# Kernel optimization log

Hardware: AMD Instinct MI355X
Metric: run time of the kernel (lower is better)

The kernel has to match this reference:

```python
import jax, jax.numpy as jnp
import numpy as np

N = 20000       # nodes
E = 100000      # edges
STEPS = 4
ND = 128        # node feature dim
ED = 128        # edge feature dim
NIN = 128       # node input dim
EIN = 291       # edge input dim (2 + 17*17)
H = 64          # mpn edge-mlp hidden


def _lin(x, w, b):
    return x @ w + b


def setup_inputs():
    key = jax.random.key(0)
    ks = jax.random.split(key, 16)

    def w(k, i, o):
        return (jax.random.normal(k, (i, o), jnp.float32) / np.float32(np.sqrt(i)))

    d = {}
    d["x"] = jax.random.normal(ks[0], (N, NIN), jnp.float32)
    d["edge_attr"] = jax.random.normal(ks[1], (E, EIN), jnp.float32)
    d["edge_index"] = jax.random.randint(ks[2], (2, E), 0, N, jnp.int32)
    # node embedding MLP: NIN -> 128 -> ND (ReLU between, none after last)
    d["new0"] = w(ks[3], NIN, 128); d["neb0"] = jnp.zeros(128, jnp.float32)
    d["new1"] = w(ks[4], 128, ND); d["neb1"] = jnp.zeros(ND, jnp.float32)
    # edge embedding MLP: EIN -> 64 -> ED
    d["eew0"] = w(ks[5], EIN, 64); d["eeb0"] = jnp.zeros(64, jnp.float32)
    d["eew1"] = w(ks[6], 64, ED); d["eeb1"] = jnp.zeros(ED, jnp.float32)
    # MPN edge MLP (skip=True): 2*(2*ND) + 2*ED = 768 -> 64 -> ED, ReLU after each
    d["mew0"] = w(ks[7], 4 * ND + 2 * ED, H); d["meb0"] = jnp.zeros(H, jnp.float32)
    d["mew1"] = w(ks[8], H, ED); d["meb1"] = jnp.zeros(ED, jnp.float32)
    # MPN node MLP: 2*ND + ED = 384 -> ND, ReLU
    d["mnw0"] = w(ks[9], 2 * ND + ED, ND); d["mnb0"] = jnp.zeros(ND, jnp.float32)
    # classification MLP: ED -> 64 -> 32 -> 1
    d["cw0"] = w(ks[10], ED, 64); d["cb0"] = jnp.zeros(64, jnp.float32)
    d["cw1"] = w(ks[11], 64, 32); d["cb1"] = jnp.zeros(32, jnp.float32)
    d["cw2"] = w(ks[12], 32, 1); d["cb2"] = jnp.zeros(1, jnp.float32)
    return d


def reference(x, edge_attr, edge_index,
              new0, neb0, new1, neb1,
              eew0, eeb0, eew1, eeb1,
              mew0, meb0, mew1, meb1,
              mnw0, mnb0,
              cw0, cb0, cw1, cb1, cw2, cb2):
    relu = jax.nn.relu
    j, i = edge_index[0], edge_index[1]  # j: source, i: target

    nf = _lin(relu(_lin(x, new0, neb0)), new1, neb1)          # [N, ND]
    ef = _lin(relu(_lin(edge_attr, eew0, eeb0)), eew1, eeb1)  # [E, ED]
    nf0, ef0 = nf, ef

    for _ in range(STEPS):
        # skip connections: concat initial features
        nfc = jnp.concatenate([nf0, nf], axis=1)  # [N, 2*ND]
        efc = jnp.concatenate([ef0, ef], axis=1)  # [E, 2*ED]
        x_i = nfc[i]  # [E, 2*ND] target
        x_j = nfc[j]  # [E, 2*ND] source
        # edge update MLP (ReLU after both layers)
        h = relu(_lin(jnp.concatenate([x_i, x_j, efc], axis=1), mew0, meb0))
        ef = relu(_lin(h, mew1, meb1))  # [E, ED]
        # message: mlp_node([x_i, edge_attr_new]) aggregated at target i
        msg = relu(_lin(jnp.concatenate([x_i, ef], axis=1), mnw0, mnb0))  # [E, ND]
        nf = jax.ops.segment_sum(msg, i, num_segments=N)  # [N, ND]

    out = relu(_lin(ef, cw0, cb0))
    out = relu(_lin(out, cw1, cb1))
    out = _lin(out, cw2, cb2)  # [E, 1]
    return out
```

## Files before the change

kernel.cpp:

```cpp
#include <hip/hip_runtime.h>
#include <hip/hip_bf16.h>

#define ND 128
#define ED 128
#define NIN 128
#define EIN 291
#define KPAD 320
#define HH 64
#define TM 32
#define TS 64
#define GSE 768
#define MAXGE 3

typedef __attribute__((ext_vector_type(8))) short short8;
typedef __attribute__((ext_vector_type(4))) float float4_;

__device__ __forceinline__ unsigned short f2bf(float f)
{
    union { float f; unsigned u; } v; v.f = f;
    unsigned u = v.u;
    unsigned r = (u + 0x7FFFu + ((u >> 16) & 1u)) >> 16;
    return (unsigned short)r;
}
__device__ __forceinline__ float bf2f(unsigned short s)
{
    union { unsigned u; float f; } v; v.u = ((unsigned)s) << 16;
    return v.f;
}

template<int T, int KC, int K>
__device__ __forceinline__ void stage_frags(const unsigned short* __restrict__ src,
                                            unsigned short* __restrict__ wreg,
                                            int t, int k0)
{
    constexpr int TOT = T * KC * 64;
#pragma unroll
    for (int it = 0; it < TOT / 256; it++) {
        int idx = it * 256 + t;
        int f = idx >> 6, l = idx & 63;
        int col = (f / KC) * 16 + (l & 15);
        int k = (f % KC) * 32 + ((l >> 4) * 8);
        *(short8*)&wreg[idx * 8] = *(const short8*)&src[(size_t)col * K + k0 + k];
    }
}
#define FRAG(wreg, f, lane) (*(const short8*)&(wreg)[(((f) << 6) + (lane)) * 8])

__global__ __launch_bounds__(256) void zero_k(float* __restrict__ p, int n4)
{
    int idx = blockIdx.x * 256 + threadIdx.x;
    if (idx < n4) ((float4*)p)[idx] = make_float4(0.f, 0.f, 0.f, 0.f);
}

__global__ __launch_bounds__(256) void f2bfz_k(float* __restrict__ src,
                                               unsigned short* __restrict__ dst, int n4)
{
    int idx = blockIdx.x * 256 + threadIdx.x;
    if (idx < n4) {
        float4 v = ((const float4*)src)[idx];
        unsigned lo = (unsigned)f2bf(v.x) | ((unsigned)f2bf(v.y) << 16);
        unsigned hi = (unsigned)f2bf(v.z) | ((unsigned)f2bf(v.w) << 16);
        ((uint2*)dst)[idx] = make_uint2(lo, hi);
        ((float4*)src)[idx] = make_float4(0.f, 0.f, 0.f, 0.f);
    }
}

__global__ __launch_bounds__(256) void wprep_k(
    const float* __restrict__ mew0, const float* __restrict__ mew1, const float* __restrict__ mnw0,
    const float* __restrict__ eew0, const float* __restrict__ eew1, const float* __restrict__ cw0,
    const float* __restrict__ new0, const float* __restrict__ new1,
    unsigned short* __restrict__ w0T, unsigned short* __restrict__ w1T,
    unsigned short* __restrict__ wmT, unsigned short* __restrict__ w0eT,
    unsigned short* __restrict__ w1eT, unsigned short* __restrict__ cw0T,
    unsigned short* __restrict__ w0nT, unsigned short* __restrict__ w1nT)
{
    int idx = blockIdx.x * 256 + threadIdx.x;
    if (idx < 49152) {
        int c = idx / 768, k = idx % 768;
        w0T[idx] = f2bf(mew0[k * 64 + c]);
    } else if (idx < 57344) {
        int j = idx - 49152; int c = j / 64, k = j % 64;
        w1T[j] = f2bf(mew1[k * 128 + c]);
    } else if (idx < 106496) {
        int j = idx - 57344; int c = j / 384, k = j % 384;
        wmT[j] = f2bf(mnw0[k * 128 + c]);
    } else if (idx < 126976) {
        int j = idx - 106496; int c = j / KPAD, k = j % KPAD;
        w0eT[j] = (k < EIN) ? f2bf(eew0[k * 64 + c]) : (unsigned short)0;
    } else if (idx < 135168) {
        int j = idx - 126976; int c = j / 64, k = j % 64;
        w1eT[j] = f2bf(eew1[k * 128 + c]);
    } else if (idx < 143360) {
        int j = idx - 135168; int c = j / 128, k = j % 128;
        cw0T[j] = f2bf(cw0[k * 64 + c]);
    } else if (idx < 159744) {
        int j = idx - 143360; int c = j / 128, k = j % 128;
        w0nT[j] = f2bf(new0[k * 128 + c]);
    } else if (idx < 176128) {
        int j = idx - 159744; int c = j / 128, k = j % 128;
        w1nT[j] = f2bf(new1[k * 128 + c]);
    }
}

__global__ __launch_bounds__(256) void node_embed_k(
    const float* __restrict__ x,
    const unsigned short* __restrict__ w0nT, const float* __restrict__ b0,
    const unsigned short* __restrict__ w1nT, const float* __restrict__ b1,
    unsigned short* __restrict__ nf0_bf, unsigned short* __restrict__ nf_bf, int N)
{
    const int t = threadIdx.x;
    const int n0 = blockIdx.x * TM;
    __shared__ unsigned short wreg[8192];
    __shared__ unsigned short xin[TM][130];
    __shared__ unsigned short h_bf[TM][130];

#pragma unroll
    for (int it = 0; it < 4; it++) {
        int idx = it * 256 + t;
        int r = idx >> 5, c4 = idx & 31;
        int node = n0 + r; if (node >= N) node = N - 1;
        float4 v = *(const float4*)(x + (size_t)node * NIN + c4 * 4);
        unsigned lo = (unsigned)f2bf(v.x) | ((unsigned)f2bf(v.y) << 16);
        unsigned hi = (unsigned)f2bf(v.z) | ((unsigned)f2bf(v.w) << 16);
        *(uint2*)&xin[r][c4 * 4] = make_uint2(lo, hi);
    }

    const int w = t >> 6, lane = t & 63, quad = lane >> 4, n16 = lane & 15;
    const int m = w & 1, nh = w >> 1;

    float4_ acc[4];
#pragma unroll
    for (int q = 0; q < 4; q++) acc[q] = (float4_){0.f, 0.f, 0.f, 0.f};
#pragma unroll
    for (int hf = 0; hf < 2; hf++) {
        stage_frags<8, 2, 128>(w0nT, wreg, t, hf * 64);
        __syncthreads();
#pragma unroll
        for (int kc = 0; kc < 2; kc++) {
            short8 a = *(const short8*)&xin[m * 16 + n16][hf * 64 + kc * 32 + quad * 8];
#pragma unroll
            for (int tt = 0; tt < 4; tt++) {
                short8 b = FRAG(wreg, (nh * 4 + tt) * 2 + kc, lane);
                acc[tt] = __builtin_amdgcn_mfma_f32_16x16x32_bf16(a, b, acc[tt], 0, 0, 0);
            }
        }
        __syncthreads();
    }
#pragma unroll
    for (int tt = 0; tt < 4; tt++) {
        int c = nh * 64 + tt * 16 + n16;
        float bias = b0[c];
#pragma unroll
        for (int r4 = 0; r4 < 4; r4++)
            h_bf[m * 16 + quad * 4 + r4][c] = f2bf(fmaxf(acc[tt][r4] + bias, 0.f));
    }
    __syncthreads();

    float4_ acc2[4];
#pragma unroll
    for (int q = 0; q < 4; q++) acc2[q] = (float4_){0.f, 0.f, 0.f, 0.f};
#pragma unroll
    for (int hf = 0; hf < 2; hf++) {
        stage_frags<8, 2, 128>(w1nT, wreg, t, hf * 64);
        __syncthreads();
#pragma unroll
        for (int kc = 0; kc < 2; kc++) {
            short8 a = *(const short8*)&h_bf[m * 16 + n16][hf * 64 + kc * 32 + quad * 8];
#pragma unroll
            for (int tt = 0; tt < 4; tt++) {
                short8 b = FRAG(wreg, (nh * 4 + tt) * 2 + kc, lane);
                acc2[tt] = __builtin_amdgcn_mfma_f32_16x16x32_bf16(a, b, acc2[tt], 0, 0, 0);
            }
        }
        __syncthreads();
    }
#pragma unroll
    for (int tt = 0; tt < 4; tt++) {
        int c = nh * 64 + tt * 16 + n16;
        float bias = b1[c];
#pragma unroll
        for (int r4 = 0; r4 < 4; r4++) {
            int row = m * 16 + quad * 4 + r4;
            int node = n0 + row;
            if (node < N) {
                unsigned short v = f2bf(acc2[tt][r4] + bias);
                nf0_bf[(size_t)node * ND + c] = v;
                nf_bf[(size_t)node * ND + c] = v;
            }
        }
    }
}

__global__ __launch_bounds__(256, 3) void edge_embed_k(
    const float* __restrict__ ea,
    const unsigned short* __restrict__ w0eT, const float* __restrict__ b0,
    const unsigned short* __restrict__ w1eT, const float* __restrict__ b1,
    unsigned short* __restrict__ ef0_bf, unsigned short* __restrict__ ef_bf,
    int E, int ntiles)
{
    const int t = threadIdx.x;
    __shared__ unsigned short w0reg[10240];
    __shared__ unsigned short w1reg[8192];
    __shared__ unsigned short hsl[4][16 * 66];

    const int w = t >> 6, lane = t & 63, quad = lane >> 4, n16 = lane & 15;

    stage_frags<8, 2, 64>(w1eT, w1reg, t, 0);

    int ng = 0;
    int tile[MAXGE];
#pragma unroll
    for (int g = 0; g < MAXGE; g++) {
        int tl = blockIdx.x + g * GSE;
        if (tl < ntiles) { tile[g] = tl; ng = g + 1; }
        else tile[g] = 0;
    }

    float4_ accL[MAXGE][4];
#pragma unroll
    for (int g = 0; g < MAXGE; g++)
#pragma unroll
        for (int q = 0; q < 4; q++) accL[g][q] = (float4_){0.f, 0.f, 0.f, 0.f};

#pragma unroll
    for (int hf = 0; hf < 2; hf++) {
        __syncthreads();
        stage_frags<4, 5, KPAD>(w0eT, w0reg, t, hf * 160);
        __syncthreads();
#pragma unroll
        for (int g = 0; g < MAXGE; g++) {
            if (g < ng) {
                int e = tile[g] * 64 + w * 16 + n16; if (e >= E) e = E - 1;
                const float* src = ea + (size_t)e * EIN;
#pragma unroll
                for (int kc = 0; kc < 5; kc++) {
                    int k = hf * 160 + kc * 32 + quad * 8;
                    union { short8 s; uint4 u; } av;
                    if (k + 8 <= EIN) {
                        float4 v0 = *(const float4*)(src + k);
                        float4 v1 = *(const float4*)(src + k + 4);
                        av.u.x = (unsigned)f2bf(v0.x) | ((unsigned)f2bf(v0.y) << 16);
                        av.u.y = (unsigned)f2bf(v0.z) | ((unsigned)f2bf(v0.w) << 16);
                        av.u.z = (unsigned)f2bf(v1.x) | ((unsigned)f2bf(v1.y) << 16);
                        av.u.w = (unsigned)f2bf(v1.z) | ((unsigned)f2bf(v1.w) << 16);
                    } else {
                        unsigned short vv[8];
#pragma unroll
                        for (int j = 0; j < 8; j++)
                            vv[j] = (k + j < EIN) ? f2bf(src[k + j]) : (unsigned short)0;
                        av.u.x = (unsigned)vv[0] | ((unsigned)vv[1] << 16);
                        av.u.y = (unsigned)vv[2] | ((unsigned)vv[3] << 16);
                        av.u.z = (unsigned)vv[4] | ((unsigned)vv[5] << 16);
                        av.u.w = (unsigned)vv[6] | ((unsigned)vv[7] << 16);
                    }
#pragma unroll
                    for (int tt = 0; tt < 4; tt++) {
                        short8 b = FRAG(w0reg, tt * 5 + kc, lane);
                        accL[g][tt] = __builtin_amdgcn_mfma_f32_16x16x32_bf16(av.s, b, accL[g][tt], 0, 0, 0);
                    }
                }
            }
        }
    }

#pragma unroll
    for (int g = 0; g < MAXGE; g++) {
        if (g < ng) {
#pragma unroll
            for (int tt = 0; tt < 4; tt++) {
                int c = tt * 16 + n16;
                float bias = b0[c];
#pragma unroll
                for (int r4 = 0; r4 < 4; r4++)
                    hsl[w][(quad * 4 + r4) * 66 + c] = f2bf(fmaxf(accL[g][tt][r4] + bias, 0.f));
            }
            float4_ acc2[8];
#pragma unroll
            for (int q = 0; q < 8; q++) acc2[q] = (float4_){0.f, 0.f, 0.f, 0.f};
#pragma unroll
            for (int kc = 0; kc < 2; kc++) {
                short8 a2 = *(const short8*)&hsl[w][n16 * 66 + kc * 32 + quad * 8];
#pragma unroll
                for (int tt = 0; tt < 8; tt++)
                    acc2[tt] = __builtin_amdgcn_mfma_f32_16x16x32_bf16(
                        a2, FRAG(w1reg, tt * 2 + kc, lane), acc2[tt], 0, 0, 0);
            }
#pragma unroll
            for (int tt = 0; tt < 8; tt++) {
                int c = tt * 16 + n16;
                float bias = b1[c];
#pragma unroll
                for (int r4 = 0; r4 < 4; r4++) {
                    int e = tile[g] * 64 + w * 16 + quad * 4 + r4;
                    if (e < E) {
                        unsigned short v = f2bf(acc2[tt][r4] + bias);
                        ef0_bf[(size_t)e * ED + c] = v;
                        ef_bf[(size_t)e * ED + c] = v;
                    }
                }
            }
        }
    }
}

__global__ __launch_bounds__(256, 3) void edge_step_k(
    const int* __restrict__ srcj, const int* __restrict__ tgti,
    const unsigned short* __restrict__ nf0_bf, const unsigned short* __restrict__ nf_bf,
    const unsigned short* __restrict__ ef0_bf, unsigned short* __restrict__ ef_bf,
    float* __restrict__ nfn,
    const unsigned short* __restrict__ w0T, const float* __restrict__ meb0,
    const unsigned short* __restrict__ w1T, const float* __restrict__ meb1,
    const unsigned short* __restrict__ wmT, const float* __restrict__ mnb0, int E)
{
    const int t = threadIdx.x;
    const int e0 = blockIdx.x * TS;
    __shared__ unsigned short wreg[8192];
    __shared__ unsigned short h_bf[TS][66];
    __shared__ unsigned short efn_bf[TS][130];
    __shared__ int sidx[TS];

    if (t < TS) { int e = e0 + t; if (e >= E) e = E - 1; sidx[t] = tgti[e]; }

    const int w = t >> 6, lane = t & 63, quad = lane >> 4, n16 = lane & 15;
    const int erow = w * 16 + n16;
    int ec = e0 + erow; if (ec >= E) ec = E - 1;
    const int ti = tgti[ec], sj = srcj[ec];

    short8 areg[24];
    {
        const unsigned short* pAs[6] = {
            nf0_bf + (size_t)ti * ND + quad * 8,
            nf_bf  + (size_t)ti * ND + quad * 8,
            nf0_bf + (size_t)sj * ND + quad * 8,
            nf_bf  + (size_t)sj * ND + quad * 8,
            ef0_bf + (size_t)ec * ED + quad * 8,
            ef_bf  + (size_t)ec * ED + quad * 8 };
#pragma unroll
        for (int f = 0; f < 24; f++)
            areg[f] = *(const short8*)(pAs[f >> 2] + (f & 3) * 32);
    }

    float4_ accL[4];
#pragma unroll
    for (int q = 0; q < 4; q++) accL[q] = (float4_){0.f, 0.f, 0.f, 0.f};
#pragma unroll
    for (int hf = 0; hf < 6; hf++) {
        stage_frags<4, 4, 768>(w0T, wreg, t, hf * 128);
        __syncthreads();
#pragma unroll
        for (int kc = 0; kc < 4; kc++) {
#pragma unroll
            for (int tt = 0; tt < 4; tt++) {
                short8 b = FRAG(wreg, tt * 4 + kc, lane);
                accL[tt] = __builtin_amdgcn_mfma_f32_16x16x32_bf16(areg[hf * 4 + kc], b, accL[tt], 0, 0, 0);
            }
        }
        __syncthreads();
    }
#pragma unroll
    for (int tt = 0; tt < 4; tt++) {
        int c = tt * 16 + n16;
        float bias = meb0[c];
#pragma unroll
        for (int r4 = 0; r4 < 4; r4++)
            h_bf[w * 16 + quad * 4 + r4][c] = f2bf(fmaxf(accL[tt][r4] + bias, 0.f));
    }
    __syncthreads();

    stage_frags<8, 2, 64>(w1T, wreg, t, 0);
    __syncthreads();
    {
        float4_ acc[8];
#pragma unroll
        for (int q = 0; q < 8; q++) acc[q] = (float4_){0.f, 0.f, 0.f, 0.f};
#pragma unroll
        for (int kc = 0; kc < 2; kc++) {
            short8 a = *(const short8*)&h_bf[w * 16 + n16][kc * 32 + quad * 8];
#pragma unroll
            for (int tt = 0; tt < 8; tt++) {
                short8 b = FRAG(wreg, tt * 2 + kc, lane);
                acc[tt] = __builtin_amdgcn_mfma_f32_16x16x32_bf16(a, b, acc[tt], 0, 0, 0);
            }
        }
#pragma unroll
        for (int tt = 0; tt < 8; tt++) {
            int c = tt * 16 + n16;
            float bias = meb1[c];
#pragma unroll
            for (int r4 = 0; r4 < 4; r4++) {
                int row = w * 16 + quad * 4 + r4;
                unsigned short v = f2bf(fmaxf(acc[tt][r4] + bias, 0.f));
                efn_bf[row][c] = v;
                int e = e0 + row;
                if (e < E) ef_bf[(size_t)e * ED + c] = v;
            }
        }
    }
    __syncthreads();

    float4_ accM[8];
#pragma unroll
    for (int q = 0; q < 8; q++) accM[q] = (float4_){0.f, 0.f, 0.f, 0.f};
#pragma unroll
    for (int hf = 0; hf < 6; hf++) {
        stage_frags<8, 2, 384>(wmT, wreg, t, hf * 64);
        __syncthreads();
#pragma unroll
        for (int kc = 0; kc < 2; kc++) {
            int kk = hf * 2 + kc;
            short8 a;
            if (kk < 8) a = areg[kk];
            else        a = *(const short8*)&efn_bf[erow][(kk - 8) * 32 + quad * 8];
#pragma unroll
            for (int tt = 0; tt < 8; tt++) {
                short8 b = FRAG(wreg, tt * 2 + kc, lane);
                accM[tt] = __builtin_amdgcn_mfma_f32_16x16x32_bf16(a, b, accM[tt], 0, 0, 0);
            }
        }
        __syncthreads();
    }
#pragma unroll
    for (int tt = 0; tt < 8; tt++) {
        int c = tt * 16 + n16;
        float bias = mnb0[c];
#pragma unroll
        for (int r4 = 0; r4 < 4; r4++) {
            int row = w * 16 + quad * 4 + r4;
            int e = e0 + row;
            if (e < E)
                atomicAdd(&nfn[(size_t)sidx[row] * ND + c],
                          fmaxf(accM[tt][r4] + bias, 0.f));
        }
    }
}

__global__ __launch_bounds__(256) void classify_k(
    const unsigned short* __restrict__ ef_bf,
    const unsigned short* __restrict__ cw0T, const float* __restrict__ cb0,
    const float* __restrict__ cw1, const float* __restrict__ cb1,
    const float* __restrict__ cw2, const float* __restrict__ cb2,
    float* __restrict__ out, int E)
{
    const int t = threadIdx.x;
    const int e0 = blockIdx.x * TM;
    __shared__ unsigned short h0_bf[TM][66];
    __shared__ float h1[TM][33];

    const int w = t >> 6, lane = t & 63, quad = lane >> 4, n16 = lane & 15;
    const int m = w & 1;
    const int erow = m * 16 + n16;
    int ec = e0 + erow; if (ec >= E) ec = E - 1;
    const unsigned short* pa = ef_bf + (size_t)ec * ED + quad * 8;

    {
        const int cb = (w >> 1) * 32;
        float4_ acc0 = {0.f, 0.f, 0.f, 0.f}, acc1 = acc0;
        const unsigned short* b0p = cw0T + (size_t)(cb + n16) * 128 + quad * 8;
        const unsigned short* b1p = b0p + (size_t)16 * 128;
#pragma unroll
        for (int kc = 0; kc < 4; kc++) {
            short8 a  = *(const short8*)(pa + kc * 32);
            short8 bb0 = *(const short8*)(b0p + kc * 32);
            short8 bb1 = *(const short8*)(b1p + kc * 32);
            acc0 = __builtin_amdgcn_mfma_f32_16x16x32_bf16(a, bb0, acc0, 0, 0, 0);
            acc1 = __builtin_amdgcn_mfma_f32_16x16x32_bf16(a, bb1, acc1, 0, 0, 0);
        }
#pragma unroll
        for (int t2 = 0; t2 < 2; t2++) {
            int c = cb + t2 * 16 + n16;
            float bias = cb0[c];
            float4_ ac = t2 ? acc1 : acc0;
#pragma unroll
            for (int r4 = 0; r4 < 4; r4++)
                h0_bf[m * 16 + quad * 4 + r4][c] = f2bf(fmaxf(ac[r4] + bias, 0.f));
        }
    }
    __syncthreads();

    {
        int c = t & 31;
        int rbase = (t >> 5) * 4;
#pragma unroll
        for (int q = 0; q < 4; q++) {
            int r = rbase + q;
            float acc = cb1[c];
#pragma unroll 8
            for (int k = 0; k < 64; k++) acc += bf2f(h0_bf[r][k]) * cw1[k * 32 + c];
            h1[r][c] = fmaxf(acc, 0.f);
        }
    }
    __syncthreads();

    if (t < TM) {
        int e = e0 + t;
        if (e < E) {
            float a = cb2[0];
#pragma unroll
            for (int k = 0; k < 32; k++) a += h1[t][k] * cw2[k];
            out[e] = a;
        }
    }
}

extern "C" void kernel_launch(void* const* d_in, const int* in_sizes, int n_in,
                              void* d_out, int out_size, void* d_ws, size_t ws_size,
                              hipStream_t stream)
{
    const float* x    = (const float*)d_in[0];
    const float* ea   = (const float*)d_in[1];
    const int*   eidx = (const int*)d_in[2];
    const float* new0 = (const float*)d_in[3];  const float* neb0 = (const float*)d_in[4];
    const float* new1 = (const float*)d_in[5];  const float* neb1 = (const float*)d_in[6];
    const float* eew0 = (const float*)d_in[7];  const float* eeb0 = (const float*)d_in[8];
    const float* eew1 = (const float*)d_in[9];  const float* eeb1 = (const float*)d_in[10];
    const float* mew0 = (const float*)d_in[11]; const float* meb0 = (const float*)d_in[12];
    const float* mew1 = (const float*)d_in[13]; const float* meb1 = (const float*)d_in[14];
    const float* mnw0 = (const float*)d_in[15]; const float* mnb0 = (const float*)d_in[16];
    const float* cw0  = (const float*)d_in[17]; const float* cb0  = (const float*)d_in[18];
    const float* cw1  = (const float*)d_in[19]; const float* cb1  = (const float*)d_in[20];
    const float* cw2  = (const float*)d_in[21]; const float* cb2  = (const float*)d_in[22];

    const int N = in_sizes[0] / NIN;
    const int E = in_sizes[2] / 2;
    const int* srcj = eidx;
    const int* tgti = eidx + E;

    char* wsb = (char*)d_ws;
    float* nfn = (float*)wsb;
    unsigned short* nf0_bf = (unsigned short*)(nfn + (size_t)N * ND);
    unsigned short* nf_bf  = nf0_bf + (size_t)N * ND;
    unsigned short* ef0_bf = nf_bf + (size_t)N * ND;
    unsigned short* ef_bf  = ef0_bf + (size_t)E * ED;
    unsigned short* w0T  = ef_bf + (size_t)E * ED;
    unsigned short* w1T  = w0T + 49152;
    unsigned short* wmT  = w1T + 8192;
    unsigned short* w0eT = wmT + 49152;
    unsigned short* w1eT = w0eT + 64 * KPAD;
    unsigned short* cw0T = w1eT + 8192;
    unsigned short* w0nT = cw0T + 8192;
    unsigned short* w1nT = w0nT + 16384;

    const int eblocks32 = (E + TM - 1) / TM;
    const int nblocks32 = (N + TM - 1) / TM;
    const int ntiles64 = (E + 63) / 64;

    wprep_k<<<(176128 + 255) / 256, 256, 0, stream>>>(mew0, mew1, mnw0, eew0, eew1, cw0,
                                                      new0, new1,
                                                      w0T, w1T, wmT, w0eT, w1eT, cw0T,
                                                      w0nT, w1nT);
    node_embed_k<<<nblocks32, 256, 0, stream>>>(x, w0nT, neb0, w1nT, neb1,
                                                nf0_bf, nf_bf, N);
    edge_embed_k<<<GSE, 256, 0, stream>>>(ea, w0eT, eeb0, w1eT, eeb1,
                                          ef0_bf, ef_bf, E, ntiles64);

    const int n4 = (N * ND) / 4;
    const int zgrid = (n4 + 255) / 256;
    zero_k<<<zgrid, 256, 0, stream>>>(nfn, n4);

    for (int s = 0; s < 4; s++) {
        edge_step_k<<<ntiles64, 256, 0, stream>>>(srcj, tgti, nf0_bf, nf_bf,
                                                  ef0_bf, ef_bf, nfn,
                                                  w0T, meb0, w1T, meb1, wmT, mnb0, E);
        f2bfz_k<<<zgrid, 256, 0, stream>>>(nfn, nf_bf, n4);
    }

    classify_k<<<eblocks32, 256, 0, stream>>>(ef_bf, cw0T, cb0, cw1, cb1, cw2, cb2,
                                              (float*)d_out, E);
}
```

Measured before the change: 786.1 us.

## Replace atomic scatter-add with CSR gather aggregation and skip unused final message

Builds a CSR index of edges grouped by target node (histogram, single-block scan, scatter) once per call. The edge step now writes bf16 messages to a buffer, and a separate gather kernel sums each node's incoming messages, replacing fp32 atomicAdd into a node buffer and the convert-and-zero pass. The last step skips the node-message MLP entirely, since its aggregate is never used by the classifier. The cost is an extra message round-trip through memory, a serial single-block scan, and bf16 rounding of messages before summation.

```diff
diff --git a/kernel.cpp b/kernel.cpp
--- a/kernel.cpp
+++ b/kernel.cpp
@@ -51,17 +51,65 @@
     if (idx < n4) ((float4*)p)[idx] = make_float4(0.f, 0.f, 0.f, 0.f);
 }
 
-__global__ __launch_bounds__(256) void f2bfz_k(float* __restrict__ src,
-                                               unsigned short* __restrict__ dst, int n4)
-{
-    int idx = blockIdx.x * 256 + threadIdx.x;
-    if (idx < n4) {
-        float4 v = ((const float4*)src)[idx];
-        unsigned lo = (unsigned)f2bf(v.x) | ((unsigned)f2bf(v.y) << 16);
-        unsigned hi = (unsigned)f2bf(v.z) | ((unsigned)f2bf(v.w) << 16);
-        ((uint2*)dst)[idx] = make_uint2(lo, hi);
-        ((float4*)src)[idx] = make_float4(0.f, 0.f, 0.f, 0.f);
-    }
+__global__ __launch_bounds__(256) void hist_k(const int* __restrict__ tgti,
+                                              int* __restrict__ deg, int E)
+{
+    int e = blockIdx.x * 256 + threadIdx.x;
+    if (e < E) atomicAdd(&deg[tgti[e]], 1);
+}
+
+__global__ __launch_bounds__(256) void scan_k(const int* __restrict__ deg,
+                                              int* __restrict__ row_ptr,
+                                              int* __restrict__ cursor, int N, int E)
+{
+    __shared__ int part[256];
+    const int t = threadIdx.x;
+    const int chunk = (N + 255) / 256;
+    const int base = t * chunk;
+    int s = 0;
+    for (int k = 0; k < chunk; k++) { int idx = base + k; if (idx < N) s += deg[idx]; }
+    part[t] = s;
+    __syncthreads();
+    for (int off = 1; off < 256; off <<= 1) {
+        int v = (t >= off) ? part[t - off] : 0;
+        __syncthreads();
+        part[t] += v;
+        __syncthreads();
+    }
+    int run = (t == 0) ? 0 : part[t - 1];
+    for (int k = 0; k < chunk; k++) {
+        int idx = base + k;
+        if (idx < N) { row_ptr[idx] = run; cursor[idx] = run; run += deg[idx]; }
+    }
+    if (t == 255) row_ptr[N] = E;
+}
+
+__global__ __launch_bounds__(256) void scatter_k(const int* __restrict__ tgti,
+                                                 int* __restrict__ cursor,
+                                                 int* __restrict__ csr_eid, int E)
+{
+    int e = blockIdx.x * 256 + threadIdx.x;
+    if (e < E) {
+        int p = atomicAdd(&cursor[tgti[e]], 1);
+        csr_eid[p] = e;
+    }
+}
+
+__global__ __launch_bounds__(256) void agg_k(const int* __restrict__ row_ptr,
+                                             const int* __restrict__ csr_eid,
+                                             const unsigned short* __restrict__ msg,
+                                             unsigned short* __restrict__ nf_bf, int N)
+{
+    int n = blockIdx.x * 2 + (threadIdx.x >> 7);
+    int c = threadIdx.x & 127;
+    if (n >= N) return;
+    int beg = row_ptr[n], end = row_ptr[n + 1];
+    float acc = 0.f;
+    for (int k = beg; k < end; k++) {
+        int e = csr_eid[k];
+        acc += bf2f(msg[(size_t)e * ND + c]);
+    }
+    nf_bf[(size_t)n * ND + c] = f2bf(acc);
 }
 
 __global__ __launch_bounds__(256) void wprep_k(
@@ -306,19 +354,17 @@
     const int* __restrict__ srcj, const int* __restrict__ tgti,
     const unsigned short* __restrict__ nf0_bf, const unsigned short* __restrict__ nf_bf,
     const unsigned short* __restrict__ ef0_bf, unsigned short* __restrict__ ef_bf,
-    float* __restrict__ nfn,
+    unsigned short* __restrict__ msg,
     const unsigned short* __restrict__ w0T, const float* __restrict__ meb0,
     const unsigned short* __restrict__ w1T, const float* __restrict__ meb1,
-    const unsigned short* __restrict__ wmT, const float* __restrict__ mnb0, int E)
+    const unsigned short* __restrict__ wmT, const float* __restrict__ mnb0,
+    int E, int wmsg)
 {
     const int t = threadIdx.x;
     const int e0 = blockIdx.x * TS;
     __shared__ unsigned short wreg[8192];
     __shared__ unsigned short h_bf[TS][66];
     __shared__ unsigned short efn_bf[TS][130];
-    __shared__ int sidx[TS];
-
-    if (t < TS) { int e = e0 + t; if (e >= E) e = E - 1; sidx[t] = tgti[e]; }
 
     const int w = t >> 6, lane = t & 63, quad = lane >> 4, n16 = lane & 15;
     const int erow = w * 16 + n16;
@@ -397,38 +443,39 @@
     }
     __syncthreads();
 
-    float4_ accM[8];
-#pragma unroll
-    for (int q = 0; q < 8; q++) accM[q] = (float4_){0.f, 0.f, 0.f, 0.f};
-#pragma unroll
-    for (int hf = 0; hf < 6; hf++) {
-        stage_frags<8, 2, 384>(wmT, wreg, t, hf * 64);
-        __syncthreads();
-#pragma unroll
-        for (int kc = 0; kc < 2; kc++) {
-            int kk = hf * 2 + kc;
-            short8 a;
-            if (kk < 8) a = areg[kk];
-            else        a = *(const short8*)&efn_bf[erow][(kk - 8) * 32 + quad * 8];
-#pragma unroll
-            for (int tt = 0; tt < 8; tt++) {
-                short8 b = FRAG(wreg, tt * 2 + kc, lane);
-                accM[tt] = __builtin_amdgcn_mfma_f32_16x16x32_bf16(a, b, accM[tt], 0, 0, 0);
-            }
-        }
-        __syncthreads();
-    }
-#pragma unroll
-    for (int tt = 0; tt < 8; tt++) {
-        int c = tt * 16 + n16;
-        float bias = mnb0[c];
-#pragma unroll
-        for (int r4 = 0; r4 < 4; r4++) {
-            int row = w * 16 + quad * 4 + r4;
-            int e = e0 + row;
-            if (e < E)
-                atomicAdd(&nfn[(size_t)sidx[row] * ND + c],
-                          fmaxf(accM[tt][r4] + bias, 0.f));
+    if (wmsg) {
+        float4_ accM[8];
+#pragma unroll
+        for (int q = 0; q < 8; q++) accM[q] = (float4_){0.f, 0.f, 0.f, 0.f};
+#pragma unroll
+        for (int hf = 0; hf < 6; hf++) {
+            stage_frags<8, 2, 384>(wmT, wreg, t, hf * 64);
+            __syncthreads();
+#pragma unroll
+            for (int kc = 0; kc < 2; kc++) {
+                int kk = hf * 2 + kc;
+                short8 a;
+                if (kk < 8) a = areg[kk];
+                else        a = *(const short8*)&efn_bf[erow][(kk - 8) * 32 + quad * 8];
+#pragma unroll
+                for (int tt = 0; tt < 8; tt++) {
+                    short8 b = FRAG(wreg, tt * 2 + kc, lane);
+                    accM[tt] = __builtin_amdgcn_mfma_f32_16x16x32_bf16(a, b, accM[tt], 0, 0, 0);
+                }
+            }
+            __syncthreads();
+        }
+#pragma unroll
+        for (int tt = 0; tt < 8; tt++) {
+            int c = tt * 16 + n16;
+            float bias = mnb0[c];
+#pragma unroll
+            for (int r4 = 0; r4 < 4; r4++) {
+                int row = w * 16 + quad * 4 + r4;
+                int e = e0 + row;
+                if (e < E)
+                    msg[(size_t)e * ND + c] = f2bf(fmaxf(accM[tt][r4] + bias, 0.f));
+            }
         }
     }
 }
@@ -525,12 +572,12 @@
     const int* tgti = eidx + E;
 
     char* wsb = (char*)d_ws;
-    float* nfn = (float*)wsb;
-    unsigned short* nf0_bf = (unsigned short*)(nfn + (size_t)N * ND);
+    unsigned short* nf0_bf = (unsigned short*)wsb;
     unsigned short* nf_bf  = nf0_bf + (size_t)N * ND;
     unsigned short* ef0_bf = nf_bf + (size_t)N * ND;
     unsigned short* ef_bf  = ef0_bf + (size_t)E * ED;
-    unsigned short* w0T  = ef_bf + (size_t)E * ED;
+    unsigned short* msg    = ef_bf + (size_t)E * ED;
+    unsigned short* w0T  = msg + (size_t)E * ND;
     unsigned short* w1T  = w0T + 49152;
     unsigned short* wmT  = w1T + 8192;
     unsigned short* w0eT = wmT + 49152;
@@ -538,6 +585,10 @@
     unsigned short* cw0T = w1eT + 8192;
     unsigned short* w0nT = cw0T + 8192;
     unsigned short* w1nT = w0nT + 16384;
+    int* deg     = (int*)(w1nT + 16384);
+    int* cursor  = deg + N;
+    int* row_ptr = cursor + N;
+    int* csr_eid = row_ptr + (N + 4);
 
     const int eblocks32 = (E + TM - 1) / TM;
     const int nblocks32 = (N + TM - 1) / TM;
@@ -547,20 +598,24 @@
                                                       new0, new1,
                                                       w0T, w1T, wmT, w0eT, w1eT, cw0T,
                                                       w0nT, w1nT);
+
+    zero_k<<<((2 * N) / 4 + 255) / 256, 256, 0, stream>>>((float*)deg, (2 * N) / 4);
+    hist_k<<<(E + 255) / 256, 256, 0, stream>>>(tgti, deg, E);
+    scan_k<<<1, 256, 0, stream>>>(deg, row_ptr, cursor, N, E);
+    scatter_k<<<(E + 255) / 256, 256, 0, stream>>>(tgti, cursor, csr_eid, E);
+
     node_embed_k<<<nblocks32, 256, 0, stream>>>(x, w0nT, neb0, w1nT, neb1,
                                                 nf0_bf, nf_bf, N);
     edge_embed_k<<<GSE, 256, 0, stream>>>(ea, w0eT, eeb0, w1eT, eeb1,
                                           ef0_bf, ef_bf, E, ntiles64);
 
-    const int n4 = (N * ND) / 4;
-    const int zgrid = (n4 + 255) / 256;
-    zero_k<<<zgrid, 256, 0, stream>>>(nfn, n4);
-
     for (int s = 0; s < 4; s++) {
         edge_step_k<<<ntiles64, 256, 0, stream>>>(srcj, tgti, nf0_bf, nf_bf,
-                                                  ef0_bf, ef_bf, nfn,
-                                                  w0T, meb0, w1T, meb1, wmT, mnb0, E);
-        f2bfz_k<<<zgrid, 256, 0, stream>>>(nfn, nf_bf, n4);
+                                                  ef0_bf, ef_bf, msg,
+                                                  w0T, meb0, w1T, meb1, wmT, mnb0,
+                                                  E, (s < 3) ? 1 : 0);
+        if (s < 3)
+            agg_k<<<(N + 1) / 2, 256, 0, stream>>>(row_ptr, csr_eid, msg, nf_bf, N);
     }
 
     classify_k<<<eblocks32, 256, 0, stream>>>(ef_bf, cw0T, cb0, cw1, cb1, cw2, cb2,
```

Measured after the change: 780.3 us. About the same (-0.7%).
